# Optimization experiments

Measured on AMD Instinct MI355X. Metric: run time of the kernel, lower is better.

## Reference

```python
import jax, jax.numpy as jnp
import numpy as np

B, T_IN, F, NB = 32768, 3, 6, 10
H = 256
BD = H // 2            # baseline_dim
T_OUT = 5
DIN = F + H + BD       # decoder LSTMCell input size
EPS = 1e-5


def _lstm_cell(x, h, c, W_ih, W_hh, b_ih, b_hh):
    # PyTorch gate order: i, f, g, o
    z = x @ W_ih.T + h @ W_hh.T + b_ih + b_hh
    i, f, g, o = jnp.split(z, 4, axis=-1)
    c = jax.nn.sigmoid(f) * c + jax.nn.sigmoid(i) * jnp.tanh(g)
    h = jax.nn.sigmoid(o) * jnp.tanh(c)
    return h, c


def _lstm_layer(xs, W_ih, W_hh, b_ih, b_hh):
    # xs: (T, B, D_in) -> outputs (T, B, H), final (h, c)
    Bn = xs.shape[1]
    h0 = jnp.zeros((Bn, H), xs.dtype)
    c0 = jnp.zeros((Bn, H), xs.dtype)

    def step(carry, x):
        h, c = carry
        h, c = _lstm_cell(x, h, c, W_ih, W_hh, b_ih, b_hh)
        return (h, c), h

    (hT, cT), ys = jax.lax.scan(step, (h0, c0), xs)
    return ys, hT, cT


def setup_inputs() -> dict:
    key = jax.random.key(0)
    ks = jax.random.split(key, 16)
    s = 0.05
    d = {
        "cbc_input": jax.random.normal(ks[0], (B, T_IN, F), jnp.float32),
        "baseline": jax.random.normal(ks[1], (B, NB), jnp.float32),
        # encoder LSTM layer 0 / 1
        "W_ih0": jax.random.normal(ks[2], (4 * H, F), jnp.float32) * s,
        "W_hh0": jax.random.normal(ks[3], (4 * H, H), jnp.float32) * s,
        "b_ih0": jnp.zeros((4 * H,), jnp.float32),
        "b_hh0": jnp.zeros((4 * H,), jnp.float32),
        "W_ih1": jax.random.normal(ks[4], (4 * H, H), jnp.float32) * s,
        "W_hh1": jax.random.normal(ks[5], (4 * H, H), jnp.float32) * s,
        "b_ih1": jnp.zeros((4 * H,), jnp.float32),
        "b_hh1": jnp.zeros((4 * H,), jnp.float32),
        # baseline encoder: Linear + ReLU + LayerNorm
        "Wb": jax.random.normal(ks[6], (BD, NB), jnp.float32) * s,
        "bb": jnp.zeros((BD,), jnp.float32),
        "ln_g": jnp.ones((BD,), jnp.float32),
        "ln_b": jnp.zeros((BD,), jnp.float32),
        # Bahdanau attention
        "W1a": jax.random.normal(ks[7], (H, H), jnp.float32) * s,
        "b1a": jnp.zeros((H,), jnp.float32),
        "W2a": jax.random.normal(ks[8], (H, H), jnp.float32) * s,
        "b2a": jnp.zeros((H,), jnp.float32),
        "va": jax.random.normal(ks[9], (1, H), jnp.float32) * s,
        "ba": jnp.zeros((1,), jnp.float32),
        # decoder LSTMCell
        "Wd_ih": jax.random.normal(ks[10], (4 * H, DIN), jnp.float32) * s,
        "Wd_hh": jax.random.normal(ks[11], (4 * H, H), jnp.float32) * s,
        "bd_ih": jnp.zeros((4 * H,), jnp.float32),
        "bd_hh": jnp.zeros((4 * H,), jnp.float32),
        # output projection MLP
        "Wo1": jax.random.normal(ks[12], (BD, H), jnp.float32) * s,
        "bo1": jnp.zeros((BD,), jnp.float32),
        "Wo2": jax.random.normal(ks[13], (F, BD), jnp.float32) * s,
        "bo2": jnp.zeros((F,), jnp.float32),
    }
    return d


def reference(cbc_input, baseline, W_ih0, W_hh0, b_ih0, b_hh0,
              W_ih1, W_hh1, b_ih1, b_hh1, Wb, bb, ln_g, ln_b,
              W1a, b1a, W2a, b2a, va, ba,
              Wd_ih, Wd_hh, bd_ih, bd_hh, Wo1, bo1, Wo2, bo2):
    # ---- encoder (2-layer LSTM, batch_first; eval mode so no dropout) ----
    xs = jnp.swapaxes(cbc_input, 0, 1)                      # (T, B, F)
    y0, _, _ = _lstm_layer(xs, W_ih0, W_hh0, b_ih0, b_hh0)  # (T, B, H)
    y1, hT, cT = _lstm_layer(y0, W_ih1, W_hh1, b_ih1, b_hh1)
    encoder_outputs = jnp.swapaxes(y1, 0, 1)                # (B, T, H)

    # ---- baseline encoder: Linear -> ReLU -> LayerNorm ----
    z = jax.nn.relu(baseline @ Wb.T + bb)
    mu = jnp.mean(z, axis=-1, keepdims=True)
    var = jnp.mean((z - mu) ** 2, axis=-1, keepdims=True)
    baseline_repr = (z - mu) * jax.lax.rsqrt(var + EPS) * ln_g + ln_b  # (B, BD)

    enc_proj = encoder_outputs @ W2a.T + b2a                # (B, T, H) precomputed
    last_cbc0 = cbc_input[:, -1, :]                         # (B, F)

    def step(carry, _):
        h, c, last_cbc = carry
        # Bahdanau attention
        q = (h @ W1a.T + b1a)[:, None, :]                   # (B, 1, H)
        scores = jnp.tanh(q + enc_proj) @ va.T + ba         # (B, T, 1)
        weights = jax.nn.softmax(scores, axis=1)
        context = jnp.sum(weights * encoder_outputs, axis=1)  # (B, H)
        dec_in = jnp.concatenate([last_cbc, context, baseline_repr], axis=1)
        h, c = _lstm_cell(dec_in, h, c, Wd_ih, Wd_hh, bd_ih, bd_hh)
        delta = jax.nn.relu(h @ Wo1.T + bo1) @ Wo2.T + bo2
        pred = last_cbc + delta
        return (h, c, pred), pred

    _, preds = jax.lax.scan(step, (hT, cT, last_cbc0), None, length=T_OUT)
    return jnp.swapaxes(preds, 0, 1)                        # (B, 5, F)
```

## Files before the change

### kernel.cpp

```cpp
#include <hip/hip_runtime.h>

typedef unsigned short u16;
typedef __bf16 bf16x8 __attribute__((ext_vector_type(8)));
typedef float f32x4 __attribute__((ext_vector_type(4)));

#define BATCH 32768L

__device__ __forceinline__ u16 f2b(float f) {
  union { float f; unsigned int u; } v; v.f = f;
  unsigned int r = v.u + 0x7fffu + ((v.u >> 16) & 1u);
  return (u16)(r >> 16);
}
__device__ __forceinline__ float b2f(u16 h) {
  union { unsigned int u; float f; } v; v.u = ((unsigned int)h) << 16;
  return v.f;
}
__device__ __forceinline__ float sigf(float x) { return 1.f / (1.f + __expf(-x)); }
__device__ __forceinline__ float tanh_f(float x) { return 2.f / (1.f + __expf(-2.f * x)) - 1.f; }

__device__ __forceinline__ void gload16(const void* g, void* l) {
  __builtin_amdgcn_global_load_lds((const __attribute__((address_space(1))) unsigned int*)g,
                                   (__attribute__((address_space(3))) unsigned int*)l,
                                   16, 0, 0);
}

struct PrepP {
  const float* s[9]; u16* d[9]; int sc[9]; int dc[9]; long n[9];
  const float* ba[3]; const float* bb_[3]; float* bo[3];
};

__global__ void prep_kernel(PrepP p, long cvtTotal, long total) {
  for (long i = (long)blockIdx.x * blockDim.x + threadIdx.x; i < total;
       i += (long)gridDim.x * blockDim.x) {
    if (i < cvtTotal) {
      long off = i; int sg = 0;
      while (off >= p.n[sg]) { off -= p.n[sg]; ++sg; }
      long r = off / p.dc[sg]; int c = (int)(off - r * p.dc[sg]);
      p.d[sg][off] = (c < p.sc[sg]) ? f2b(p.s[sg][r * (long)p.sc[sg] + c]) : (u16)0;
    } else {
      long j = i - cvtTotal; int sg = (int)(j >> 10); int k = (int)(j & 1023);
      p.bo[sg][k] = p.ba[sg][k] + p.bb_[sg][k];
    }
  }
}

template <int EPI, int NG>
__global__ __launch_bounds__(256, 2)
void mfma_gemm4(const u16* __restrict__ A1, long lda1, int K1,
                const u16* __restrict__ W1, int wld1,
                const u16* __restrict__ A2, long lda2, int K2,
                const u16* __restrict__ W2, int wld2,
                int gs, int ys, const float* __restrict__ bias,
                u16* __restrict__ out0, int ldo, int relu,
                const float* __restrict__ cprev, float* __restrict__ cout,
                u16* __restrict__ hout, int ldh)
{
  __shared__ u16 As[3][128 * 32];
  __shared__ u16 Bs[3][NG * 64 * 32];
  const int tid = threadIdx.x;
  const int l = tid & 63, w = tid >> 6;
  const long bm = (long)blockIdx.x * 128;
  const int yb = blockIdx.y;

  const int nch1 = K1 >> 5;
  const int nch2 = A2 ? (K2 >> 5) : 0;
  const int nt = nch1 + nch2;

  f32x4 acc[8][NG];
#pragma unroll
  for (int rf = 0; rf < 8; ++rf)
#pragma unroll
    for (int g = 0; g < NG; ++g) acc[rf][g] = (f32x4){0.f, 0.f, 0.f, 0.f};

  const int l4q = l >> 2;
  const int swzs = ((l & 3) ^ ((l >> 2) & 3)) * 16;

  const char* pA[2];
  const char* pB[NG];
  auto initA = [&](const u16* A, long lda) {
#pragma unroll
    for (int c = 0; c < 2; ++c)
      pA[c] = (const char*)A + ((bm + w * 32 + c * 16 + l4q) * lda) * 2 + swzs;
  };
  auto initB = [&](const u16* W, int wld) {
#pragma unroll
    for (int c = 0; c < NG; ++c) {
      const int brow = w * (NG * 16) + c * 16 + l4q;
      const long wrow = (long)(brow >> 6) * gs + (long)yb * ys + (brow & 63);
      pB[c] = (const char*)W + (wrow * (long)wld) * 2 + swzs;
    }
  };
  auto stage = [&](int buf) {
#pragma unroll
    for (int c = 0; c < 2; ++c) {
      gload16(pA[c], &As[buf][(w * 32 + c * 16) * 32]);
      pA[c] += 64;
    }
#pragma unroll
    for (int c = 0; c < NG; ++c) {
      gload16(pB[c], &Bs[buf][(w * (NG * 16) + c * 16) * 32]);
      pB[c] += 64;
    }
  };

  initA(A1, lda1);
  initB(W1, wld1);
  stage(0);
  if (A2 && nch1 == 1) { initA(A2, lda2); initB(W2, wld2); }
  if (nt > 1) stage(1);

  const int rb = l & 15;
  const int koff = ((l >> 4) ^ (l & 3)) * 8;
  int bufR = 0, bufS = 2;
  for (int ch = 0; ch < nt; ++ch) {
    if (ch + 1 < nt) {
      asm volatile("s_waitcnt vmcnt(%0)\n\ts_barrier" :: "i"(2 + NG) : "memory");
    } else {
      asm volatile("s_waitcnt vmcnt(0)\n\ts_barrier" ::: "memory");
    }
    const int s = ch + 2;
    if (s < nt) {
      if (A2 && s == nch1) { initA(A2, lda2); initB(W2, wld2); }
      stage(bufS);
    }
    const u16* Ab = As[bufR];
    const u16* Bb = Bs[bufR];
    bf16x8 af[8];
#pragma unroll
    for (int rf = 0; rf < 8; ++rf)
      af[rf] = *(const bf16x8*)&Ab[(rf * 16 + rb) * 32 + koff];
#pragma unroll
    for (int g = 0; g < NG; ++g) {
      bf16x8 bfr = *(const bf16x8*)&Bb[(g * 64 + w * 16 + rb) * 32 + koff];
#pragma unroll
      for (int rf = 0; rf < 8; ++rf)
        acc[rf][g] = __builtin_amdgcn_mfma_f32_16x16x32_bf16(af[rf], bfr, acc[rf][g], 0, 0, 0);
    }
    bufR = (bufR == 2) ? 0 : bufR + 1;
    bufS = (bufS == 2) ? 0 : bufS + 1;
  }

  const int colb = l & 15;
  const int rq = l >> 4;
  if constexpr (EPI == 0) {
#pragma unroll
    for (int g = 0; g < NG; ++g) {
      const int wrow = g * gs + yb * ys + w * 16 + colb;
      const float bi = bias[wrow];
#pragma unroll
      for (int rf = 0; rf < 8; ++rf) {
#pragma unroll
        for (int r = 0; r < 4; ++r) {
          const long row = bm + rf * 16 + rq * 4 + r;
          float vv = acc[rf][g][r] + bi;
          if (relu) vv = fmaxf(vv, 0.f);
          out0[row * (long)ldo + wrow] = f2b(vv);
        }
      }
    }
  } else {
    const int cb = yb * 64 + w * 16 + colb;
    const float b_i = bias[cb];
    const float b_f = bias[256 + cb];
    const float b_g = bias[512 + cb];
    const float b_o = bias[768 + cb];
#pragma unroll
    for (int rf = 0; rf < 8; ++rf) {
#pragma unroll
      for (int r = 0; r < 4; ++r) {
        const long row = bm + rf * 16 + rq * 4 + r;
        const float zi = acc[rf][0][r] + b_i;
        const float zf = acc[rf][1][r] + b_f;
        const float zg = acc[rf][2][r] + b_g;
        const float zo = acc[rf][3][r] + b_o;
        const float cp = cprev ? cprev[row * 256 + cb] : 0.f;
        const float cn = sigf(zf) * cp + sigf(zi) * tanh_f(zg);
        const float hn = sigf(zo) * tanh_f(cn);
        cout[row * 256 + cb] = cn;
        hout[row * (long)ldh + cb] = f2b(hn);
      }
    }
  }
}

__global__ __launch_bounds__(256)
void front_kernel(const float* __restrict__ cbc, const float* __restrict__ baseline,
                  const float* __restrict__ Wb, const float* __restrict__ bb,
                  const float* __restrict__ ln_g, const float* __restrict__ ln_b,
                  u16* __restrict__ dec_in, u16* __restrict__ xbf)
{
  __shared__ float wbs[1280];
  __shared__ float bbs[128], lgs[128], lbs[128];
  const int tid = threadIdx.x;
  for (int i = tid; i < 1280; i += 256) wbs[i] = Wb[i];
  if (tid < 128) { bbs[tid] = bb[tid]; lgs[tid] = ln_g[tid]; lbs[tid] = ln_b[tid]; }
  __syncthreads();
  const int l = tid & 63, w = tid >> 6;
  const long row = (long)blockIdx.x * 4 + w;
#pragma unroll
  for (int e = l; e < 96; e += 64) {
    const int t = e >> 5, c = e & 31;
    xbf[(row * 3 + t) * 32 + c] = (c < 6) ? f2b(cbc[row * 18 + t * 6 + c]) : (u16)0;
  }
  if (l < 6) dec_in[row * 416 + l] = f2b(cbc[row * 18 + 12 + l]);
  else if (l < 32) dec_in[row * 416 + 390 + (l - 6)] = 0;
  float bl[10];
#pragma unroll
  for (int k = 0; k < 10; ++k) bl[k] = baseline[row * 10 + k];
  const int c0 = l, c1 = l + 64;
  float z0 = bbs[c0], z1 = bbs[c1];
#pragma unroll
  for (int k = 0; k < 10; ++k) { z0 += bl[k] * wbs[c0 * 10 + k]; z1 += bl[k] * wbs[c1 * 10 + k]; }
  z0 = fmaxf(z0, 0.f); z1 = fmaxf(z1, 0.f);
  float s = z0 + z1, sq = z0 * z0 + z1 * z1;
#pragma unroll
  for (int m = 32; m; m >>= 1) { s += __shfl_xor(s, m); sq += __shfl_xor(sq, m); }
  const float mu = s * (1.f / 128.f);
  const float var = sq * (1.f / 128.f) - mu * mu;
  const float rs = rsqrtf(var + 1e-5f);
  dec_in[row * 416 + 262 + c0] = f2b((z0 - mu) * rs * lgs[c0] + lbs[c0]);
  dec_in[row * 416 + 262 + c1] = f2b((z1 - mu) * rs * lgs[c1] + lbs[c1]);
}

__global__ __launch_bounds__(256)
void attn_kernel(const u16* __restrict__ q, const u16* __restrict__ ep,
                 const u16* __restrict__ eo, const float* __restrict__ va,
                 const float* __restrict__ ba, u16* __restrict__ dec_in)
{
  const int tid = threadIdx.x;
  const int l = tid & 63, w = tid >> 6;
  const long row = (long)blockIdx.x * 4 + w;
  const int c = l * 4;
  float qv[4], vav[4];
  {
    ushort4 qu = *(const ushort4*)&q[row * 256 + c];
    qv[0] = b2f(qu.x); qv[1] = b2f(qu.y); qv[2] = b2f(qu.z); qv[3] = b2f(qu.w);
    float4 vv = *(const float4*)&va[c];
    vav[0] = vv.x; vav[1] = vv.y; vav[2] = vv.z; vav[3] = vv.w;
  }
  float s[3];
#pragma unroll
  for (int t = 0; t < 3; ++t) {
    ushort4 eu = *(const ushort4*)&ep[row * 768 + t * 256 + c];
    float p = tanh_f(qv[0] + b2f(eu.x)) * vav[0]
            + tanh_f(qv[1] + b2f(eu.y)) * vav[1]
            + tanh_f(qv[2] + b2f(eu.z)) * vav[2]
            + tanh_f(qv[3] + b2f(eu.w)) * vav[3];
#pragma unroll
    for (int m = 32; m; m >>= 1) p += __shfl_xor(p, m);
    s[t] = p + ba[0];
  }
  const float mx = fmaxf(s[0], fmaxf(s[1], s[2]));
  const float e0 = __expf(s[0] - mx), e1 = __expf(s[1] - mx), e2 = __expf(s[2] - mx);
  const float inv = 1.f / (e0 + e1 + e2);
  const float w0 = e0 * inv, w1 = e1 * inv, w2 = e2 * inv;
  const ushort4 a0 = *(const ushort4*)&eo[row * 768 + 0 * 256 + c];
  const ushort4 a1 = *(const ushort4*)&eo[row * 768 + 1 * 256 + c];
  const ushort4 a2 = *(const ushort4*)&eo[row * 768 + 2 * 256 + c];
  u16* dp = &dec_in[row * 416 + 6 + c];
  dp[0] = f2b(w0 * b2f(a0.x) + w1 * b2f(a1.x) + w2 * b2f(a2.x));
  dp[1] = f2b(w0 * b2f(a0.y) + w1 * b2f(a1.y) + w2 * b2f(a2.y));
  dp[2] = f2b(w0 * b2f(a0.z) + w1 * b2f(a1.z) + w2 * b2f(a2.z));
  dp[3] = f2b(w0 * b2f(a0.w) + w1 * b2f(a1.w) + w2 * b2f(a2.w));
}

__global__ __launch_bounds__(256)
void delta_kernel(const u16* __restrict__ t1, const float* __restrict__ Wo2,
                  const float* __restrict__ bo2, const float* __restrict__ lastp, int lstride,
                  float* __restrict__ outp, int ostride, u16* __restrict__ dec_in)
{
  __shared__ float w2s[768];
  __shared__ float part[64][4][6];
  const int tid = threadIdx.x;
  for (int i = tid; i < 768; i += 256) w2s[i] = Wo2[i];
  __syncthreads();
  const int rw = tid >> 2, q = tid & 3;
  const long row = (long)blockIdx.x * 64 + rw;
  float p[6] = {0.f, 0.f, 0.f, 0.f, 0.f, 0.f};
  const u16* tp = &t1[row * 128 + q * 32];
#pragma unroll
  for (int it = 0; it < 4; ++it) {
    int4 chunk = *(const int4*)&tp[it * 8];
    const u16* cu = (const u16*)&chunk;
#pragma unroll
    for (int e = 0; e < 8; ++e) {
      const float tv = b2f(cu[e]);
      const int k = q * 32 + it * 8 + e;
#pragma unroll
      for (int j = 0; j < 6; ++j) p[j] += tv * w2s[j * 128 + k];
    }
  }
#pragma unroll
  for (int j = 0; j < 6; ++j) part[rw][q][j] = p[j];
  __syncthreads();
  if (tid < 64) {
    const long r2 = (long)blockIdx.x * 64 + tid;
#pragma unroll
    for (int j = 0; j < 6; ++j) {
      const float d = bo2[j] + part[tid][0][j] + part[tid][1][j] + part[tid][2][j] + part[tid][3][j];
      const float pr = lastp[r2 * lstride + j] + d;
      outp[r2 * ostride + j] = pr;
      dec_in[r2 * 416 + j] = f2b(pr);
    }
  }
}

extern "C" void kernel_launch(void* const* d_in, const int* in_sizes, int n_in,
                              void* d_out, int out_size, void* d_ws, size_t ws_size,
                              hipStream_t stream) {
  const float* cbc   = (const float*)d_in[0];
  const float* base  = (const float*)d_in[1];
  const float* W_ih0 = (const float*)d_in[2];
  const float* W_hh0 = (const float*)d_in[3];
  const float* b_ih0 = (const float*)d_in[4];
  const float* b_hh0 = (const float*)d_in[5];
  const float* W_ih1 = (const float*)d_in[6];
  const float* W_hh1 = (const float*)d_in[7];
  const float* b_ih1 = (const float*)d_in[8];
  const float* b_hh1 = (const float*)d_in[9];
  const float* Wb    = (const float*)d_in[10];
  const float* bb    = (const float*)d_in[11];
  const float* ln_g  = (const float*)d_in[12];
  const float* ln_b  = (const float*)d_in[13];
  const float* W1a   = (const float*)d_in[14];
  const float* b1a   = (const float*)d_in[15];
  const float* W2a   = (const float*)d_in[16];
  const float* b2a   = (const float*)d_in[17];
  const float* va    = (const float*)d_in[18];
  const float* ba    = (const float*)d_in[19];
  const float* Wd_ih = (const float*)d_in[20];
  const float* Wd_hh = (const float*)d_in[21];
  const float* bd_ih = (const float*)d_in[22];
  const float* bd_hh = (const float*)d_in[23];
  const float* Wo1   = (const float*)d_in[24];
  const float* bo1   = (const float*)d_in[25];
  const float* Wo2   = (const float*)d_in[26];
  const float* bo2   = (const float*)d_in[27];
  float* out = (float*)d_out;
  (void)in_sizes; (void)n_in; (void)out_size;

  unsigned char* wsb = (unsigned char*)d_ws;
  size_t off = 0;
  auto alloc = [&](size_t bytes) -> void* {
    void* p = wsb + off;
    off += (bytes + 255) & ~(size_t)255;
    return p;
  };
  u16* wih0b = (u16*)alloc(1024 * 32 * 2);
  u16* whh0b = (u16*)alloc(1024 * 256 * 2);
  u16* wih1b = (u16*)alloc(1024 * 256 * 2);
  u16* whh1b = (u16*)alloc(1024 * 256 * 2);
  u16* wdihb = (u16*)alloc(1024 * 416 * 2);
  u16* wdhhb = (u16*)alloc(1024 * 256 * 2);
  u16* w1ab  = (u16*)alloc(256 * 256 * 2);
  u16* w2ab  = (u16*)alloc(256 * 256 * 2);
  u16* wo1b  = (u16*)alloc(128 * 256 * 2);
  float* bsum0 = (float*)alloc(1024 * 4);
  float* bsum1 = (float*)alloc(1024 * 4);
  float* bsumd = (float*)alloc(1024 * 4);

  const long perRow = 6656;
  long avail = (long)ws_size - (long)off - 32768;
  long R = avail > 0 ? avail / perRow : 128;
  R &= ~127L;
  if (R > BATCH) R = BATCH;
  if (R < 128) R = 128;

  u16* xbf    = (u16*)alloc((size_t)R * 96 * 2);
  u16* y0     = (u16*)alloc((size_t)R * 768 * 2);
  u16* y1     = (u16*)alloc((size_t)R * 768 * 2);
  float* cbuf = (float*)alloc((size_t)R * 256 * 4);
  u16* hdec0  = (u16*)alloc((size_t)R * 256 * 2);
  u16* hdec1  = (u16*)alloc((size_t)R * 256 * 2);
  u16* qt1    = (u16*)alloc((size_t)R * 256 * 2);
  u16* dec_in = (u16*)alloc((size_t)R * 416 * 2);

  {
    PrepP p;
    const float* ss[9] = {W_ih0, W_hh0, W_ih1, W_hh1, Wd_ih, Wd_hh, W1a, W2a, Wo1};
    u16* dd[9]         = {wih0b, whh0b, wih1b, whh1b, wdihb, wdhhb, w1ab, w2ab, wo1b};
    int scv[9]         = {6, 256, 256, 256, 390, 256, 256, 256, 256};
    int dcv[9]         = {32, 256, 256, 256, 416, 256, 256, 256, 256};
    long rows[9]       = {1024, 1024, 1024, 1024, 1024, 1024, 256, 256, 128};
    long cvtTotal = 0;
    for (int i = 0; i < 9; ++i) {
      p.s[i] = ss[i]; p.d[i] = dd[i]; p.sc[i] = scv[i]; p.dc[i] = dcv[i];
      p.n[i] = rows[i] * dcv[i]; cvtTotal += p.n[i];
    }
    p.ba[0] = b_ih0; p.bb_[0] = b_hh0; p.bo[0] = bsum0;
    p.ba[1] = b_ih1; p.bb_[1] = b_hh1; p.bo[1] = bsum1;
    p.ba[2] = bd_ih; p.bb_[2] = bd_hh; p.bo[2] = bsumd;
    prep_kernel<<<dim3(2048), dim3(256), 0, stream>>>(p, cvtTotal, cvtTotal + 3072);
  }

  const dim3 blk(256);

  for (long r0 = 0; r0 < BATCH; r0 += R) {
    const long Rc = (BATCH - r0 < R) ? (BATCH - r0) : R;
    const unsigned nb = (unsigned)(Rc / 128);
    const dim3 gcell(nb, 4);
    const float* cbc_c  = cbc + r0 * 18;
    const float* base_c = base + r0 * 10;
    float* out_c = out + r0 * 30;

    front_kernel<<<dim3((unsigned)(Rc / 4)), blk, 0, stream>>>(
        cbc_c, base_c, Wb, bb, ln_g, ln_b, dec_in, xbf);

    for (int t = 0; t < 3; ++t) {
      const u16* a2 = t ? (y0 + (t - 1) * 256) : nullptr;
      mfma_gemm4<1, 4><<<gcell, blk, 0, stream>>>(
          xbf + t * 32, 96, 32, wih0b, 32,
          a2, 768, 256, whh0b, 256,
          256, 64, bsum0,
          nullptr, 0, 0,
          (t ? cbuf : nullptr), cbuf, y0 + t * 256, 768);
    }
    for (int t = 0; t < 3; ++t) {
      const u16* a2 = t ? (y1 + (t - 1) * 256) : nullptr;
      mfma_gemm4<1, 4><<<gcell, blk, 0, stream>>>(
          y0 + t * 256, 768, 256, wih1b, 256,
          a2, 768, 256, whh1b, 256,
          256, 64, bsum1,
          nullptr, 0, 0,
          (t ? cbuf : nullptr), cbuf, y1 + t * 256, 768);
    }
    mfma_gemm4<0, 4><<<dim3(nb * 3, 1), blk, 0, stream>>>(
        y1, 256, 256, w2ab, 256,
        nullptr, 0, 0, nullptr, 0,
        64, 0, b2a,
        y0, 256, 0,
        nullptr, nullptr, nullptr, 0);

    const u16* hcur = y1 + 2 * 256; long hld = 768;
    for (int s = 0; s < 5; ++s) {
      mfma_gemm4<0, 2><<<dim3(nb, 2), blk, 0, stream>>>(
          hcur, hld, 256, w1ab, 256,
          nullptr, 0, 0, nullptr, 0,
          64, 128, b1a,
          qt1, 256, 0,
          nullptr, nullptr, nullptr, 0);
      attn_kernel<<<dim3((unsigned)(Rc / 4)), blk, 0, stream>>>(qt1, y0, y1, va, ba, dec_in);
      u16* hnext = (s & 1) ? hdec1 : hdec0;
      mfma_gemm4<1, 4><<<gcell, blk, 0, stream>>>(
          dec_in, 416, 416, wdihb, 416,
          hcur, hld, 256, wdhhb, 256,
          256, 64, bsumd,
          nullptr, 0, 0,
          cbuf, cbuf, hnext, 256);
      hcur = hnext; hld = 256;
      mfma_gemm4<0, 2><<<dim3(nb, 1), blk, 0, stream>>>(
          hcur, 256, 256, wo1b, 256,
          nullptr, 0, 0, nullptr, 0,
          64, 0, bo1,
          qt1, 128, 1,
          nullptr, nullptr, nullptr, 0);
      const float* lastp = (s == 0) ? (cbc_c + 12) : (out_c + (long)(s - 1) * 6);
      const int lstr = (s == 0) ? 18 : 30;
      delta_kernel<<<dim3((unsigned)(Rc / 64)), blk, 0, stream>>>(
          qt1, Wo2, bo2, lastp, lstr, out_c + (long)s * 6, 30, dec_in);
    }
  }
}
```

Baseline: 1.038 ms.

## Widen GEMM tiles to 256 rows, double-buffer, transpose cell state, fast math

```diff
diff --git a/kernel.cpp b/kernel.cpp
--- a/kernel.cpp
+++ b/kernel.cpp
@@ -15,8 +15,13 @@
   union { unsigned int u; float f; } v; v.u = ((unsigned int)h) << 16;
   return v.f;
 }
-__device__ __forceinline__ float sigf(float x) { return 1.f / (1.f + __expf(-x)); }
-__device__ __forceinline__ float tanh_f(float x) { return 2.f / (1.f + __expf(-2.f * x)) - 1.f; }
+__device__ __forceinline__ float rcpf(float x) { return __builtin_amdgcn_rcpf(x); }
+__device__ __forceinline__ float sigf(float x) {
+  return rcpf(1.f + __builtin_amdgcn_exp2f(-1.442695041f * x));
+}
+__device__ __forceinline__ float tanh_f(float x) {
+  return 1.f - 2.f * rcpf(1.f + __builtin_amdgcn_exp2f(2.885390082f * x));
+}
 
 __device__ __forceinline__ void gload16(const void* g, void* l) {
   __builtin_amdgcn_global_load_lds((const __attribute__((address_space(1))) unsigned int*)g,
@@ -44,39 +49,49 @@
   }
 }
 
-template <int EPI, int NG>
-__global__ __launch_bounds__(256, 2)
-void mfma_gemm4(const u16* __restrict__ A1, long lda1, int K1,
+template <int EPI, int NG, int WR>
+__global__ __launch_bounds__(WR == 1 ? 256 : 512, 4)
+void mfma_gemm5(const u16* __restrict__ A1, long lda1, int K1,
                 const u16* __restrict__ W1, int wld1,
                 const u16* __restrict__ A2, long lda2, int K2,
                 const u16* __restrict__ W2, int wld2,
                 int gs, int ys, const float* __restrict__ bias,
                 u16* __restrict__ out0, int ldo, int relu,
-                const float* __restrict__ cprev, float* __restrict__ cout,
+                const float* __restrict__ cprev, float* __restrict__ cout, long cR,
                 u16* __restrict__ hout, int ldh)
 {
-  __shared__ u16 As[3][128 * 32];
-  __shared__ u16 Bs[3][NG * 64 * 32];
+  __shared__ u16 As[2][128 * WR * 32];
+  __shared__ u16 Bs[2][NG * 64 * 32];
   const int tid = threadIdx.x;
   const int l = tid & 63, w = tid >> 6;
-  const long bm = (long)blockIdx.x * 128;
+  const int wr = w >> 2, wc = w & 3;
+  const long bm = (long)blockIdx.x * (128 * WR);
   const int yb = blockIdx.y;
 
   const int nch1 = K1 >> 5;
   const int nch2 = A2 ? (K2 >> 5) : 0;
   const int nt = nch1 + nch2;
 
+  const int colb = l & 15, rq = l >> 4;
+  const int cb = yb * ys + wc * 16 + colb;
+
   f32x4 acc[8][NG];
-#pragma unroll
-  for (int rf = 0; rf < 8; ++rf)
-#pragma unroll
-    for (int g = 0; g < NG; ++g) acc[rf][g] = (f32x4){0.f, 0.f, 0.f, 0.f};
+  {
+    float bw[NG];
+#pragma unroll
+    for (int g = 0; g < NG; ++g) bw[g] = bias[g * gs + yb * ys + wc * 16 + colb];
+#pragma unroll
+    for (int rf = 0; rf < 8; ++rf)
+#pragma unroll
+      for (int g = 0; g < NG; ++g) acc[rf][g] = (f32x4){bw[g], bw[g], bw[g], bw[g]};
+  }
 
   const int l4q = l >> 2;
   const int swzs = ((l & 3) ^ ((l >> 2) & 3)) * 16;
+  constexpr int NBS = NG / WR;
 
   const char* pA[2];
-  const char* pB[NG];
+  const char* pB[NBS];
   auto initA = [&](const u16* A, long lda) {
 #pragma unroll
     for (int c = 0; c < 2; ++c)
@@ -84,8 +99,8 @@
   };
   auto initB = [&](const u16* W, int wld) {
 #pragma unroll
-    for (int c = 0; c < NG; ++c) {
-      const int brow = w * (NG * 16) + c * 16 + l4q;
+    for (int c = 0; c < NBS; ++c) {
+      const int brow = (w * NBS + c) * 16 + l4q;
       const long wrow = (long)(brow >> 6) * gs + (long)yb * ys + (brow & 63);
       pB[c] = (const char*)W + (wrow * (long)wld) * 2 + swzs;
     }
@@ -97,8 +112,8 @@
       pA[c] += 64;
     }
 #pragma unroll
-    for (int c = 0; c < NG; ++c) {
-      gload16(pB[c], &Bs[buf][(w * (NG * 16) + c * 16) * 32]);
+    for (int c = 0; c < NBS; ++c) {
+      gload16(pB[c], &Bs[buf][((w * NBS + c) * 16) * 32]);
       pB[c] += 64;
     }
   };
@@ -106,79 +121,78 @@
   initA(A1, lda1);
   initB(W1, wld1);
   stage(0);
-  if (A2 && nch1 == 1) { initA(A2, lda2); initB(W2, wld2); }
-  if (nt > 1) stage(1);
+
+  float4 creg[8];
+  if constexpr (EPI == 1) {
+    if (cprev) {
+      const float* cpb = cprev + (size_t)cb * cR + bm + wr * 128 + rq * 4;
+#pragma unroll
+      for (int rf = 0; rf < 8; ++rf)
+        creg[rf] = *(const float4*)(cpb + rf * 16);
+    } else {
+#pragma unroll
+      for (int rf = 0; rf < 8; ++rf) creg[rf] = (float4){0.f, 0.f, 0.f, 0.f};
+    }
+  }
 
   const int rb = l & 15;
   const int koff = ((l >> 4) ^ (l & 3)) * 8;
-  int bufR = 0, bufS = 2;
+  int cur = 0;
   for (int ch = 0; ch < nt; ++ch) {
+    __syncthreads();
     if (ch + 1 < nt) {
-      asm volatile("s_waitcnt vmcnt(%0)\n\ts_barrier" :: "i"(2 + NG) : "memory");
-    } else {
-      asm volatile("s_waitcnt vmcnt(0)\n\ts_barrier" ::: "memory");
-    }
-    const int s = ch + 2;
-    if (s < nt) {
-      if (A2 && s == nch1) { initA(A2, lda2); initB(W2, wld2); }
-      stage(bufS);
-    }
-    const u16* Ab = As[bufR];
-    const u16* Bb = Bs[bufR];
+      if (A2 && ch + 1 == nch1) { initA(A2, lda2); initB(W2, wld2); }
+      stage(cur ^ 1);
+    }
+    const u16* Ab = As[cur];
+    const u16* Bb = Bs[cur];
     bf16x8 af[8];
 #pragma unroll
     for (int rf = 0; rf < 8; ++rf)
-      af[rf] = *(const bf16x8*)&Ab[(rf * 16 + rb) * 32 + koff];
+      af[rf] = *(const bf16x8*)&Ab[(wr * 128 + rf * 16 + rb) * 32 + koff];
 #pragma unroll
     for (int g = 0; g < NG; ++g) {
-      bf16x8 bfr = *(const bf16x8*)&Bb[(g * 64 + w * 16 + rb) * 32 + koff];
+      bf16x8 bfr = *(const bf16x8*)&Bb[(g * 64 + wc * 16 + rb) * 32 + koff];
 #pragma unroll
       for (int rf = 0; rf < 8; ++rf)
         acc[rf][g] = __builtin_amdgcn_mfma_f32_16x16x32_bf16(af[rf], bfr, acc[rf][g], 0, 0, 0);
     }
-    bufR = (bufR == 2) ? 0 : bufR + 1;
-    bufS = (bufS == 2) ? 0 : bufS + 1;
-  }
-
-  const int colb = l & 15;
-  const int rq = l >> 4;
+    cur ^= 1;
+  }
+
+  const long r0 = bm + wr * 128;
   if constexpr (EPI == 0) {
 #pragma unroll
     for (int g = 0; g < NG; ++g) {
-      const int wrow = g * gs + yb * ys + w * 16 + colb;
-      const float bi = bias[wrow];
+      const int wrow = g * gs + yb * ys + wc * 16 + colb;
 #pragma unroll
       for (int rf = 0; rf < 8; ++rf) {
 #pragma unroll
         for (int r = 0; r < 4; ++r) {
-          const long row = bm + rf * 16 + rq * 4 + r;
-          float vv = acc[rf][g][r] + bi;
+          float vv = acc[rf][g][r];
           if (relu) vv = fmaxf(vv, 0.f);
-          out0[row * (long)ldo + wrow] = f2b(vv);
+          out0[(r0 + rf * 16 + rq * 4 + r) * (long)ldo + wrow] = f2b(vv);
         }
       }
     }
   } else {
-    const int cb = yb * 64 + w * 16 + colb;
-    const float b_i = bias[cb];
-    const float b_f = bias[256 + cb];
-    const float b_g = bias[512 + cb];
-    const float b_o = bias[768 + cb];
+    float* cob = cout + (size_t)cb * cR + r0 + rq * 4;
 #pragma unroll
     for (int rf = 0; rf < 8; ++rf) {
+      float4 cn4;
 #pragma unroll
       for (int r = 0; r < 4; ++r) {
-        const long row = bm + rf * 16 + rq * 4 + r;
-        const float zi = acc[rf][0][r] + b_i;
-        const float zf = acc[rf][1][r] + b_f;
-        const float zg = acc[rf][2][r] + b_g;
-        const float zo = acc[rf][3][r] + b_o;
-        const float cp = cprev ? cprev[row * 256 + cb] : 0.f;
+        const float zi = acc[rf][0][r];
+        const float zf = acc[rf][1][r];
+        const float zg = acc[rf][2][r];
+        const float zo = acc[rf][3][r];
+        const float cp = ((const float*)&creg[rf])[r];
         const float cn = sigf(zf) * cp + sigf(zi) * tanh_f(zg);
         const float hn = sigf(zo) * tanh_f(cn);
-        cout[row * 256 + cb] = cn;
-        hout[row * (long)ldh + cb] = f2b(hn);
+        ((float*)&cn4)[r] = cn;
+        hout[(r0 + rf * 16 + rq * 4 + r) * (long)ldh + cb] = f2b(hn);
       }
+      *(float4*)(cob + rf * 16) = cn4;
     }
   }
 }
@@ -252,7 +266,7 @@
   }
   const float mx = fmaxf(s[0], fmaxf(s[1], s[2]));
   const float e0 = __expf(s[0] - mx), e1 = __expf(s[1] - mx), e2 = __expf(s[2] - mx);
-  const float inv = 1.f / (e0 + e1 + e2);
+  const float inv = rcpf(e0 + e1 + e2);
   const float w0 = e0 * inv, w1 = e1 * inv, w2 = e2 * inv;
   const ushort4 a0 = *(const ushort4*)&eo[row * 768 + 0 * 256 + c];
   const ushort4 a1 = *(const ushort4*)&eo[row * 768 + 1 * 256 + c];
@@ -361,10 +375,10 @@
 
   const long perRow = 6656;
   long avail = (long)ws_size - (long)off - 32768;
-  long R = avail > 0 ? avail / perRow : 128;
-  R &= ~127L;
+  long R = avail > 0 ? avail / perRow : 256;
+  R &= ~255L;
   if (R > BATCH) R = BATCH;
-  if (R < 128) R = 128;
+  if (R < 256) R = 256;
 
   u16* xbf    = (u16*)alloc((size_t)R * 96 * 2);
   u16* y0     = (u16*)alloc((size_t)R * 768 * 2);
@@ -393,70 +407,71 @@
     prep_kernel<<<dim3(2048), dim3(256), 0, stream>>>(p, cvtTotal, cvtTotal + 3072);
   }
 
-  const dim3 blk(256);
+  const dim3 blk1(256), blk2(512);
 
   for (long r0 = 0; r0 < BATCH; r0 += R) {
     const long Rc = (BATCH - r0 < R) ? (BATCH - r0) : R;
-    const unsigned nb = (unsigned)(Rc / 128);
-    const dim3 gcell(nb, 4);
+    const unsigned nb256 = (unsigned)(Rc / 256);
+    const unsigned nb128 = (unsigned)(Rc / 128);
+    const dim3 gcell(nb256, 4);
     const float* cbc_c  = cbc + r0 * 18;
     const float* base_c = base + r0 * 10;
     float* out_c = out + r0 * 30;
 
-    front_kernel<<<dim3((unsigned)(Rc / 4)), blk, 0, stream>>>(
+    front_kernel<<<dim3((unsigned)(Rc / 4)), blk1, 0, stream>>>(
         cbc_c, base_c, Wb, bb, ln_g, ln_b, dec_in, xbf);
 
     for (int t = 0; t < 3; ++t) {
       const u16* a2 = t ? (y0 + (t - 1) * 256) : nullptr;
-      mfma_gemm4<1, 4><<<gcell, blk, 0, stream>>>(
+      mfma_gemm5<1, 4, 2><<<gcell, blk2, 0, stream>>>(
           xbf + t * 32, 96, 32, wih0b, 32,
           a2, 768, 256, whh0b, 256,
           256, 64, bsum0,
           nullptr, 0, 0,
-          (t ? cbuf : nullptr), cbuf, y0 + t * 256, 768);
+          (t ? cbuf : nullptr), cbuf, R, y0 + t * 256, 768);
     }
     for (int t = 0; t < 3; ++t) {
       const u16* a2 = t ? (y1 + (t - 1) * 256) : nullptr;
-      mfma_gemm4<1, 4><<<gcell, blk, 0, stream>>>(
+      mfma_gemm5<1, 4, 2><<<gcell, blk2, 0, stream>>>(
           y0 + t * 256, 768, 256, wih1b, 256,
           a2, 768, 256, whh1b, 256,
           256, 64, bsum1,
           nullptr, 0, 0,
-          (t ? cbuf : nullptr), cbuf, y1 + t * 256, 768);
-    }
-    mfma_gemm4<0, 4><<<dim3(nb * 3, 1), blk, 0, stream>>>(
+          (t ? cbuf : nullptr), cbuf, R, y1 + t * 256, 768);
+    }
+    mfma_gemm5<0, 4, 2><<<dim3(nb256 * 3, 1), blk2, 0, stream>>>(
         y1, 256, 256, w2ab, 256,
         nullptr, 0, 0, nullptr, 0,
         64, 0, b2a,
         y0, 256, 0,
-        nullptr, nullptr, nullptr, 0);
+        nullptr, nullptr, 0, nullptr, 0);
 
     const u16* hcur = y1 + 2 * 256; long hld = 768;
     for (int s = 0; s < 5; ++s) {
-      mfma_gemm4<0, 2><<<dim3(nb, 2), blk, 0, stream>>>(
+      mfma_gemm5<0, 2, 1><<<dim3(nb128, 2), blk1, 0, stream>>>(
           hcur, hld, 256, w1ab, 256,
           nullptr, 0, 0, nullptr, 0,
           64, 128, b1a,
           qt1, 256, 0,
-          nullptr, nullptr, nullptr, 0);
-      attn_kernel<<<dim3((unsigned)(Rc / 4)), blk, 0, stream>>>(qt1, y0, y1, va, ba, dec_in);
+          nullptr, nullptr, 0, nullptr, 0);
+      attn_kernel<<<dim3((unsigned)(Rc / 4)), blk1, 0, stream>>>(qt1, y0, y1, va, ba, dec_in);
       u16* hnext = (s & 1) ? hdec1 : hdec0;
-      mfma_gemm4<1, 4><<<gcell, blk, 0, stream>>>(
+      mfma_gemm5<1, 4, 2><<<gcell, blk2, 0, stream>>>(
           dec_in, 416, 416, wdihb, 416,
           hcur, hld, 256, wdhhb, 256,
           256, 64, bsumd,
           nullptr, 0, 0,
-          cbuf, cbuf, hnext, 256);
+          cbuf, cbuf, R, hnext, 256);
       hcur = hnext; hld = 256;
-      mfma_gemm4<0, 2><<<dim3(nb, 1), blk, 0, stream>>>(
+      mfma_gemm5<0, 2, 1><<<dim3(nb128, 1), blk1, 0, stream>>>(
           hcur, 256, 256, wo1b, 256,
           nullptr, 0, 0, nullptr, 0,
           64, 0, bo1,
           qt1, 128, 1,
-          nullptr, nullptr, nullptr, 0);
+          nullptr, nullptr, 0, nullptr, 0);
       const float* lastp = (s == 0) ? (cbc_c + 12) : (out_c + (long)(s - 1) * 6);
       const int lstr = (s == 0) ? 18 : 30;
-      delta_kernel<<<dim3((unsigned)(Rc / 64)), blk, 0, stream>>>(
+      delta_kernel<<<dim3((unsigned)(Rc / 64)), blk1, 0, stream>>>(
           qt1, Wo2, bo2, lastp, lstr, out_c + (long)s * 6, 30, dec_in);
     }
   }
```

Result: slower. 3.890 ms (+274.7%).
